# Kernel tuning notes

Measured on AMD Instinct MI355X. Metric: run time of the kernel, lower is better.

Reference implementation:

```python
import jax, jax.numpy as jnp
import numpy as np

N = 100_000   # total vertices
E = 1_600_000 # total directed edges
B = 64        # graphs in batch
HID = 128
DM = 256
EPS = 1e-5


def _linear_init(k, fan_in, fan_out):
    lim = 1.0 / np.sqrt(fan_in)
    kw, kb = jax.random.split(k)
    W = jax.random.uniform(kw, (fan_in, fan_out), minval=-lim, maxval=lim, dtype=jnp.float32)
    b = jax.random.uniform(kb, (fan_out,), minval=-lim, maxval=lim, dtype=jnp.float32)
    return W, b


def setup_inputs() -> dict:
    key = jax.random.key(0)
    ks = jax.random.split(key, 8)
    W_in, b_in = _linear_init(ks[0], 3, HID)
    W1, b1 = _linear_init(ks[1], HID, HID)
    W2, b2 = _linear_init(ks[2], HID, HID)
    W3, b3 = _linear_init(ks[3], HID, HID)
    W_out, b_out = _linear_init(ks[4], HID, DM)
    vertices = jax.random.normal(ks[5], (N, 3), dtype=jnp.float32)
    edge_index = jax.random.randint(ks[6], (2, E), 0, N)
    batch = jnp.sort(jax.random.randint(ks[7], (N,), 0, B))
    gamma = jnp.ones((DM,), jnp.float32)
    beta = jnp.zeros((DM,), jnp.float32)
    return dict(vertices=vertices, edge_index=edge_index, batch=batch,
                W_in=W_in, b_in=b_in, W1=W1, b1=b1, W2=W2, b2=b2, W3=W3, b3=b3,
                W_out=W_out, b_out=b_out, gamma=gamma, beta=beta)


def _gcn_conv(x, W, b, src, dst):
    # PyG GCNConv: add self-loops, sym-normalize by deg^{-1/2}, aggregate at dst.
    h = x @ W  # [N, HID]
    deg = jnp.zeros((x.shape[0],), x.dtype).at[dst].add(1.0) + 1.0  # +1 self-loop
    dinv = jax.lax.rsqrt(deg)
    msg = h[src] * (dinv[src] * dinv[dst])[:, None]       # [E, HID] gather+scale
    agg = jnp.zeros_like(h).at[dst].add(msg)               # scatter-add
    agg = agg + h * (dinv * dinv)[:, None]                 # self-loop contribution
    return agg + b


def reference(vertices, edge_index, batch, W_in, b_in, W1, b1, W2, b2, W3, b3, W_out, b_out, gamma, beta):
    src, dst = edge_index[0], edge_index[1]
    x = vertices @ W_in + b_in
    for W, b in ((W1, b1), (W2, b2), (W3, b3)):
        x = jax.nn.relu(_gcn_conv(x, W, b, src, dst))
    # global_mean_pool over batch segments
    summ = jax.ops.segment_sum(x, batch, num_segments=B)
    cnt = jax.ops.segment_sum(jnp.ones((x.shape[0], 1), x.dtype), batch, num_segments=B)
    pooled = summ / jnp.maximum(cnt, 1.0)
    y = pooled @ W_out + b_out
    mu = jnp.mean(y, axis=-1, keepdims=True)
    var = jnp.var(y, axis=-1, keepdims=True)
    return (y - mu) * jax.lax.rsqrt(var + EPS) * gamma + beta
```

## Files before the change

### kernel.cpp

```cpp
#include <hip/hip_runtime.h>

constexpr int NV = 100000;
constexpr int NE = 1600000;
constexpr int NB = 64;
constexpr int HD = 128;
constexpr int DM = 256;
#define EPSLN 1e-5f

constexpr int DPB   = 256;
constexpr int NBUCK = (NV + DPB - 1) / DPB;
constexpr int BCAP  = 8192;
constexpr int BSH   = 13;
constexpr int EPB2  = 2048;
constexpr int NEB2  = (NE + EPB2 - 1) / EPB2;
constexpr int H1B   = 1024;
constexpr int WTB   = 128;
constexpr int BDB   = (NV + 255) / 256;

typedef short bf16x8 __attribute__((ext_vector_type(8)));
typedef float f32x4 __attribute__((ext_vector_type(4)));

__device__ inline unsigned short f2b(float f) {
    union { float f; unsigned u; } x; x.f = f;
    unsigned r = x.u + 0x7FFF + ((x.u >> 16) & 1);
    return (unsigned short)(r >> 16);
}
__device__ inline float b2f(unsigned short h) {
    union { unsigned u; float f; } x; x.u = (unsigned)h << 16;
    return x.f;
}

__global__ __launch_bounds__(256) void k_init(const float* __restrict__ verts,
                                              const float* __restrict__ Win,
                                              const float* __restrict__ bin,
                                              const float* __restrict__ W1,
                                              const float* __restrict__ W2,
                                              const float* __restrict__ W3,
                                              const int* __restrict__ ei,
                                              const int* __restrict__ batch,
                                              int* __restrict__ bcursor,
                                              int* __restrict__ ebuf,
                                              unsigned short* __restrict__ Hb,
                                              unsigned short* __restrict__ Wt,
                                              int* __restrict__ gstart,
                                              int* __restrict__ gend) {
    int t = threadIdx.x;
    int bid = blockIdx.x;
    if (bid < NEB2) {
        __shared__ int h[NBUCK];
        __shared__ int lbase[NBUCK];
        for (int i = t; i < NBUCK; i += 256) h[i] = 0;
        __syncthreads();
        int base = bid * EPB2;
        int s[8], d[8], rk[8];
        #pragma unroll
        for (int j = 0; j < 8; ++j) {
            int idx = base + j * 256 + t;
            if (idx < NE) {
                s[j] = ei[idx];
                d[j] = ei[NE + idx];
                rk[j] = atomicAdd(&h[d[j] >> 8], 1);
            } else d[j] = -1;
        }
        __syncthreads();
        for (int i = t; i < NBUCK; i += 256) {
            int c = h[i];
            if (c) lbase[i] = atomicAdd(&bcursor[i], c);
        }
        __syncthreads();
        #pragma unroll
        for (int j = 0; j < 8; ++j)
            if (d[j] >= 0) {
                int b = d[j] >> 8;
                ebuf[(b << BSH) + lbase[b] + rk[j]] = (s[j] << 8) | (d[j] & 255);
            }
        return;
    }
    if (bid < NEB2 + H1B) {
        __shared__ float Wc[3 * HD];
        __shared__ float bc[HD];
        if (t < HD) {
            float w0 = 0.f, w1 = 0.f, w2 = 0.f, bv = 0.f;
            for (int k = 0; k < HD; ++k) {
                float w = W1[k * HD + t];
                w0 = fmaf(Win[k], w, w0);
                w1 = fmaf(Win[128 + k], w, w1);
                w2 = fmaf(Win[256 + k], w, w2);
                bv = fmaf(bin[k], w, bv);
            }
            Wc[t] = w0; Wc[128 + t] = w1; Wc[256 + t] = w2; bc[t] = bv;
        }
        __syncthreads();
        for (int idx = (bid - NEB2) * 256 + t; idx < NV * HD; idx += H1B * 256) {
            int v = idx >> 7, c = idx & 127;
            float a = verts[v * 3 + 0], b = verts[v * 3 + 1], d = verts[v * 3 + 2];
            Hb[idx] = f2b(bc[c] + a * Wc[c] + b * Wc[128 + c] + d * Wc[256 + c]);
        }
        return;
    }
    if (bid < NEB2 + H1B + WTB) {
        int idx = (bid - NEB2 - H1B) * 256 + t;
        if (idx < 2 * HD * HD) {
            int l = idx >> 14, r = idx & 16383;
            const float* W = (l == 0) ? W2 : W3;
            int n = r >> 7, k = r & 127;
            Wt[(l << 14) + n * HD + k] = f2b(W[k * HD + n]);
        }
        return;
    }
    int i = (bid - NEB2 - H1B - WTB) * 256 + t;
    if (i < NV) {
        int b = batch[i];
        if (i == 0 || batch[i - 1] != b) gstart[b] = i;
        int bn = (i + 1 < NV) ? batch[i + 1] : -1;
        if (bn != b) gend[b] = i + 1;
    }
}

__global__ __launch_bounds__(256) void k_bcsr(const int* __restrict__ ebuf,
                                              const int* __restrict__ bcursor,
                                              int* __restrict__ degi,
                                              float* __restrict__ dinv,
                                              int* __restrict__ rowstart,
                                              int* __restrict__ csr) {
    __shared__ int els[BCAP];
    __shared__ int h[DPB];
    __shared__ int sdata[DPB];
    int b = blockIdx.x, t = threadIdx.x, d0 = b * DPB;
    h[t] = 0;
    __syncthreads();
    int e0 = b << BSH;
    int n = bcursor[b];
    for (int i = t; i < n; i += 256) {
        int p = ebuf[e0 + i];
        if (i < BCAP) els[i] = p;
        atomicAdd(&h[p & 255], 1);
    }
    __syncthreads();
    int a = h[t];
    sdata[t] = a;
    __syncthreads();
    for (int off = 1; off < 256; off <<= 1) {
        int v = sdata[t];
        int add = (t >= off) ? sdata[t - off] : 0;
        __syncthreads();
        sdata[t] = v + add;
        __syncthreads();
    }
    int excl = (t == 0) ? 0 : sdata[t - 1];
    int v0 = d0 + t;
    if (v0 < NV) {
        rowstart[v0] = e0 + excl;
        degi[v0] = a;
        dinv[v0] = rsqrtf((float)a + 1.0f);
    }
    h[t] = e0 + excl;
    __syncthreads();
    for (int i = t; i < n; i += 256) {
        int p = (i < BCAP) ? els[i] : ebuf[e0 + i];
        int slot = atomicAdd(&h[p & 255], 1);
        csr[slot] = p >> 8;
    }
}

__global__ __launch_bounds__(256) void k_gemm_mfma(const unsigned short* __restrict__ Xb,
                                                   const unsigned short* __restrict__ Wt,
                                                   unsigned short* __restrict__ Hb) {
    __shared__ __align__(16) unsigned short Ws[128 * 132];
    __shared__ __align__(16) unsigned short hs[4][16][136];
    int t = threadIdx.x;
    {
        int row = t >> 1;
        int half = (t & 1) << 6;
        const unsigned short* src = Wt + row * HD + half;
        unsigned short* dst = &Ws[row * 132 + half];
        #pragma unroll
        for (int i = 0; i < 8; ++i)
            *(bf16x8*)(dst + i * 8) = *(const bf16x8*)(src + i * 8);
    }
    int wave = t >> 6;
    int lane = t & 63;
    int r = lane & 15;
    int g = lane >> 4;
    int row0 = blockIdx.x * 64 + wave * 16;
    int arow = row0 + r;
    bool valid = arow < NV;

    bf16x8 afrag[4];
    const unsigned short* xp = Xb + (size_t)arow * HD + g * 8;
    #pragma unroll
    for (int ks = 0; ks < 4; ++ks) {
        if (valid) afrag[ks] = *(const bf16x8*)(xp + ks * 32);
        else       afrag[ks] = bf16x8{0, 0, 0, 0, 0, 0, 0, 0};
    }
    __syncthreads();

    #pragma unroll
    for (int nt = 0; nt < 8; ++nt) {
        f32x4 acc = {0.f, 0.f, 0.f, 0.f};
        #pragma unroll
        for (int ks = 0; ks < 4; ++ks) {
            bf16x8 bfrag = *(const bf16x8*)&Ws[(nt * 16 + r) * 132 + g * 8 + ks * 32];
            acc = __builtin_amdgcn_mfma_f32_16x16x32_bf16(afrag[ks], bfrag, acc, 0, 0, 0);
        }
        #pragma unroll
        for (int j = 0; j < 4; ++j)
            hs[wave][g * 4 + j][nt * 16 + r] = f2b(acc[j]);
    }
    int row = lane >> 2;
    int grow = row0 + row;
    #pragma unroll
    for (int k = 0; k < 4; ++k) {
        int c = (lane & 3) + k * 4;
        bf16x8 val = *(const bf16x8*)&hs[wave][row][c * 8];
        if (grow < NV)
            *(bf16x8*)(Hb + (size_t)grow * HD + c * 8) = val;
    }
}

__global__ __launch_bounds__(256) void k_agg(const unsigned short* __restrict__ H,
                                             const float* __restrict__ dinv,
                                             const int* __restrict__ rowstart,
                                             const int* __restrict__ degi,
                                             const int* __restrict__ csr_src,
                                             const float* __restrict__ bias,
                                             unsigned short* __restrict__ Xo) {
    int gtid = blockIdx.x * 256 + threadIdx.x;
    int v = gtid >> 6;
    if (v >= NV) return;
    int lane = threadIdx.x & 63;
    int q = lane >> 4;
    int l4 = lane & 15;
    float di = dinv[v];
    int rs = rowstart[v], len = degi[v];
    float a[8];
    if (q == 0) {
        float sc = di * di;
        bf16x8 hv = *(const bf16x8*)(H + (size_t)v * HD + l4 * 8);
        #pragma unroll
        for (int jj = 0; jj < 8; ++jj) a[jj] = b2f((unsigned short)hv[jj]) * sc;
    } else {
        #pragma unroll
        for (int jj = 0; jj < 8; ++jj) a[jj] = 0.f;
    }
    int cnt = (len - q + 3) >> 2;
    int idx = rs + q;
    int j = 0;
    for (; j + 1 < cnt; j += 2) {
        int s0 = csr_src[idx], s1 = csr_src[idx + 4];
        idx += 8;
        float w0 = dinv[s0] * di, w1 = dinv[s1] * di;
        bf16x8 h0 = *(const bf16x8*)(H + (size_t)s0 * HD + l4 * 8);
        bf16x8 h1 = *(const bf16x8*)(H + (size_t)s1 * HD + l4 * 8);
        #pragma unroll
        for (int jj = 0; jj < 8; ++jj) {
            a[jj] = fmaf(b2f((unsigned short)h0[jj]), w0, a[jj]);
            a[jj] = fmaf(b2f((unsigned short)h1[jj]), w1, a[jj]);
        }
    }
    if (j < cnt) {
        int s0 = csr_src[idx];
        float w0 = dinv[s0] * di;
        bf16x8 h0 = *(const bf16x8*)(H + (size_t)s0 * HD + l4 * 8);
        #pragma unroll
        for (int jj = 0; jj < 8; ++jj)
            a[jj] = fmaf(b2f((unsigned short)h0[jj]), w0, a[jj]);
    }
    #pragma unroll
    for (int jj = 0; jj < 8; ++jj) {
        a[jj] += __shfl_xor(a[jj], 16);
        a[jj] += __shfl_xor(a[jj], 32);
    }
    if (q == 0) {
        bf16x8 ov;
        #pragma unroll
        for (int jj = 0; jj < 8; ++jj)
            ov[jj] = (short)f2b(fmaxf(a[jj] + bias[l4 * 8 + jj], 0.f));
        *(bf16x8*)(Xo + (size_t)v * HD + l4 * 8) = ov;
    }
}

__global__ __launch_bounds__(256) void k_pool(const unsigned short* __restrict__ X,
                                              const int* __restrict__ batch,
                                              float* __restrict__ pool) {
    constexpr int CHUNK = (NV + 2047) / 2048;
    __shared__ float lp[2][HD];
    __shared__ int binfo[2];
    int t = threadIdx.x;
    int v0 = blockIdx.x * CHUNK;
    if (v0 >= NV) return;
    int vend = min(v0 + CHUNK, NV);
    if (t < 2 * HD) ((float*)lp)[t] = 0.f;
    if (t == 0) { binfo[0] = batch[v0]; binfo[1] = batch[vend - 1]; }
    __syncthreads();
    int b0 = binfo[0], b1 = binfo[1];
    int cg = t & 15;
    int ro = t >> 4;
    if (b1 - b0 <= 1) {
        float a0[8] = {}, a1[8] = {};
        for (int v = v0 + ro; v < vend; v += 16) {
            bf16x8 x = *(const bf16x8*)(X + (size_t)v * HD + cg * 8);
            if (batch[v] == b0) {
                #pragma unroll
                for (int jj = 0; jj < 8; ++jj) a0[jj] += b2f((unsigned short)x[jj]);
            } else {
                #pragma unroll
                for (int jj = 0; jj < 8; ++jj) a1[jj] += b2f((unsigned short)x[jj]);
            }
        }
        #pragma unroll
        for (int jj = 0; jj < 8; ++jj) {
            atomicAdd(&lp[0][cg * 8 + jj], a0[jj]);
            if (b1 != b0) atomicAdd(&lp[1][cg * 8 + jj], a1[jj]);
        }
        __syncthreads();
        int slot = t >> 7, col = t & 127;
        if (slot == 0 || b1 != b0)
            atomicAdd(&pool[(slot ? b1 : b0) * HD + col], lp[slot][col]);
    } else {
        float a[8] = {};
        int cur = -1;
        for (int v = v0 + ro; v < vend; v += 16) {
            int bb = batch[v];
            if (bb != cur) {
                if (cur >= 0) {
                    #pragma unroll
                    for (int jj = 0; jj < 8; ++jj) {
                        atomicAdd(&pool[cur * HD + cg * 8 + jj], a[jj]);
                        a[jj] = 0.f;
                    }
                }
                cur = bb;
            }
            bf16x8 x = *(const bf16x8*)(X + (size_t)v * HD + cg * 8);
            #pragma unroll
            for (int jj = 0; jj < 8; ++jj) a[jj] += b2f((unsigned short)x[jj]);
        }
        if (cur >= 0) {
            #pragma unroll
            for (int jj = 0; jj < 8; ++jj)
                atomicAdd(&pool[cur * HD + cg * 8 + jj], a[jj]);
        }
    }
}

__global__ __launch_bounds__(256) void k_out(const float* __restrict__ pool,
                                             const int* __restrict__ gstart,
                                             const int* __restrict__ gend,
                                             const float* __restrict__ Wout,
                                             const float* __restrict__ bout,
                                             const float* __restrict__ gamma,
                                             const float* __restrict__ beta,
                                             float* __restrict__ out) {
    __shared__ float ps[HD];
    __shared__ float red[DM];
    int g = blockIdx.x, t = threadIdx.x;
    if (t < HD) {
        float cn = fmaxf((float)(gend[g] - gstart[g]), 1.0f);
        ps[t] = pool[g * HD + t] / cn;
    }
    __syncthreads();
    float acc = bout[t];
    #pragma unroll 8
    for (int k = 0; k < HD; ++k) acc = fmaf(ps[k], Wout[k * DM + t], acc);
    red[t] = acc; __syncthreads();
    for (int s2 = 128; s2 > 0; s2 >>= 1) {
        if (t < s2) red[t] += red[t + s2];
        __syncthreads();
    }
    float mu = red[0] * (1.0f / DM);
    __syncthreads();
    float d = acc - mu;
    red[t] = d * d; __syncthreads();
    for (int s2 = 128; s2 > 0; s2 >>= 1) {
        if (t < s2) red[t] += red[t + s2];
        __syncthreads();
    }
    float var = red[0] * (1.0f / DM);
    out[g * DM + t] = d * rsqrtf(var + EPSLN) * gamma[t] + beta[t];
}

extern "C" void kernel_launch(void* const* d_in, const int* in_sizes, int n_in,
                              void* d_out, int out_size, void* d_ws, size_t ws_size,
                              hipStream_t stream) {
    const float* verts = (const float*)d_in[0];
    const int*   ei    = (const int*)d_in[1];
    const int*   batch = (const int*)d_in[2];
    const float* Win   = (const float*)d_in[3];
    const float* bin   = (const float*)d_in[4];
    const float* W1    = (const float*)d_in[5];
    const float* b1    = (const float*)d_in[6];
    const float* W2    = (const float*)d_in[7];
    const float* b2    = (const float*)d_in[8];
    const float* W3    = (const float*)d_in[9];
    const float* b3    = (const float*)d_in[10];
    const float* Wout  = (const float*)d_in[11];
    const float* bout  = (const float*)d_in[12];
    const float* gamma = (const float*)d_in[13];
    const float* beta  = (const float*)d_in[14];
    float* out = (float*)d_out;

    char* wp = (char*)d_ws;
    auto alloc = [&](size_t bytes) -> char* {
        char* p = wp;
        wp += (bytes + 255) & ~(size_t)255;
        return p;
    };
    unsigned short* bufA = (unsigned short*)alloc((size_t)NV * HD * 2);
    unsigned short* bufB = (unsigned short*)alloc((size_t)NV * HD * 2);
    unsigned short* Wt   = (unsigned short*)alloc((size_t)2 * HD * HD * 2);
    int*   degi     = (int*)alloc((size_t)NV * 4);
    float* dinv     = (float*)alloc((size_t)NV * 4);
    int*   rowstart = (int*)alloc((size_t)NV * 4);
    int*   csr      = (int*)alloc((size_t)NBUCK * BCAP * 4);
    int*   ebuf     = (int*)alloc((size_t)NBUCK * BCAP * 4);
    size_t zb_cursor = ((size_t)NBUCK * 4 + 255) & ~(size_t)255;
    size_t zb_pool   = (size_t)NB * HD * 4;
    size_t zb_tot    = zb_cursor + zb_pool + 1024;
    char*  zblock   = alloc(zb_tot);
    int*   bcursor  = (int*)zblock;
    float* pool     = (float*)(zblock + zb_cursor);
    int*   gstart   = (int*)(zblock + zb_cursor + zb_pool);
    int*   gend     = (int*)(zblock + zb_cursor + zb_pool + 512);

    hipMemsetAsync(zblock, 0, zb_tot, stream);

    k_init<<<NEB2 + H1B + WTB + BDB, 256, 0, stream>>>(verts, Win, bin, W1, W2, W3,
                                                       ei, batch, bcursor, ebuf,
                                                       bufA, Wt, gstart, gend);
    k_bcsr<<<NBUCK, 256, 0, stream>>>(ebuf, bcursor, degi, dinv, rowstart, csr);

    int aggrid = (int)(((size_t)NV * 64 + 255) / 256);
    k_agg<<<aggrid, 256, 0, stream>>>(bufA, dinv, rowstart, degi, csr, b1, bufB);
    k_gemm_mfma<<<(NV + 63) / 64, 256, 0, stream>>>(bufB, Wt, bufA);
    k_agg<<<aggrid, 256, 0, stream>>>(bufA, dinv, rowstart, degi, csr, b2, bufB);
    k_gemm_mfma<<<(NV + 63) / 64, 256, 0, stream>>>(bufB, Wt + (size_t)HD * HD, bufA);
    k_agg<<<aggrid, 256, 0, stream>>>(bufA, dinv, rowstart, degi, csr, b3, bufB);

    k_pool<<<2048, 256, 0, stream>>>(bufB, batch, pool);
    k_out<<<NB, 256, 0, stream>>>(pool, gstart, gend, Wout, bout, gamma, beta, out);
}
```

Baseline: 340.3 us.

## Double edges per bucketing block, reuse weight LDS for GEMM staging, zero pool in init

Each edge-bucketing block now handles 4096 edges instead of 2048, which halves the number of blocks and the global cursor atomics at the cost of more registers per thread. The GEMM kernel keeps all eight accumulator tiles in registers, then reuses the weight shared buffer for output staging after a barrier, so the separate staging array is dropped and shared memory per block shrinks, which may raise occupancy. Pool zeroing moves from the memset into the init kernel, which shrinks the memset.

```diff
diff --git a/kernel.cpp b/kernel.cpp
--- a/kernel.cpp
+++ b/kernel.cpp
@@ -11,8 +11,8 @@
 constexpr int NBUCK = (NV + DPB - 1) / DPB;
 constexpr int BCAP  = 8192;
 constexpr int BSH   = 13;
-constexpr int EPB2  = 2048;
-constexpr int NEB2  = (NE + EPB2 - 1) / EPB2;
+constexpr int EPB3  = 4096;
+constexpr int NEB3  = (NE + EPB3 - 1) / EPB3;
 constexpr int H1B   = 1024;
 constexpr int WTB   = 128;
 constexpr int BDB   = (NV + 255) / 256;
@@ -43,18 +43,19 @@
                                               unsigned short* __restrict__ Hb,
                                               unsigned short* __restrict__ Wt,
                                               int* __restrict__ gstart,
-                                              int* __restrict__ gend) {
+                                              int* __restrict__ gend,
+                                              float* __restrict__ pool) {
     int t = threadIdx.x;
     int bid = blockIdx.x;
-    if (bid < NEB2) {
+    if (bid < NEB3) {
         __shared__ int h[NBUCK];
         __shared__ int lbase[NBUCK];
         for (int i = t; i < NBUCK; i += 256) h[i] = 0;
         __syncthreads();
-        int base = bid * EPB2;
-        int s[8], d[8], rk[8];
-        #pragma unroll
-        for (int j = 0; j < 8; ++j) {
+        int base = bid * EPB3;
+        int s[16], d[16], rk[16];
+        #pragma unroll
+        for (int j = 0; j < 16; ++j) {
             int idx = base + j * 256 + t;
             if (idx < NE) {
                 s[j] = ei[idx];
@@ -69,14 +70,14 @@
         }
         __syncthreads();
         #pragma unroll
-        for (int j = 0; j < 8; ++j)
+        for (int j = 0; j < 16; ++j)
             if (d[j] >= 0) {
                 int b = d[j] >> 8;
                 ebuf[(b << BSH) + lbase[b] + rk[j]] = (s[j] << 8) | (d[j] & 255);
             }
         return;
     }
-    if (bid < NEB2 + H1B) {
+    if (bid < NEB3 + H1B) {
         __shared__ float Wc[3 * HD];
         __shared__ float bc[HD];
         if (t < HD) {
@@ -91,15 +92,15 @@
             Wc[t] = w0; Wc[128 + t] = w1; Wc[256 + t] = w2; bc[t] = bv;
         }
         __syncthreads();
-        for (int idx = (bid - NEB2) * 256 + t; idx < NV * HD; idx += H1B * 256) {
+        for (int idx = (bid - NEB3) * 256 + t; idx < NV * HD; idx += H1B * 256) {
             int v = idx >> 7, c = idx & 127;
             float a = verts[v * 3 + 0], b = verts[v * 3 + 1], d = verts[v * 3 + 2];
             Hb[idx] = f2b(bc[c] + a * Wc[c] + b * Wc[128 + c] + d * Wc[256 + c]);
         }
         return;
     }
-    if (bid < NEB2 + H1B + WTB) {
-        int idx = (bid - NEB2 - H1B) * 256 + t;
+    if (bid < NEB3 + H1B + WTB) {
+        int idx = (bid - NEB3 - H1B) * 256 + t;
         if (idx < 2 * HD * HD) {
             int l = idx >> 14, r = idx & 16383;
             const float* W = (l == 0) ? W2 : W3;
@@ -108,7 +109,8 @@
         }
         return;
     }
-    int i = (bid - NEB2 - H1B - WTB) * 256 + t;
+    int i = (bid - NEB3 - H1B - WTB) * 256 + t;
+    if (i < NB * HD) pool[i] = 0.f;
     if (i < NV) {
         int b = batch[i];
         if (i == 0 || batch[i - 1] != b) gstart[b] = i;
@@ -167,7 +169,6 @@
                                                    const unsigned short* __restrict__ Wt,
                                                    unsigned short* __restrict__ Hb) {
     __shared__ __align__(16) unsigned short Ws[128 * 132];
-    __shared__ __align__(16) unsigned short hs[4][16][136];
     int t = threadIdx.x;
     {
         int row = t >> 1;
@@ -195,24 +196,29 @@
     }
     __syncthreads();
 
+    f32x4 acc[8];
     #pragma unroll
     for (int nt = 0; nt < 8; ++nt) {
-        f32x4 acc = {0.f, 0.f, 0.f, 0.f};
+        acc[nt] = f32x4{0.f, 0.f, 0.f, 0.f};
         #pragma unroll
         for (int ks = 0; ks < 4; ++ks) {
             bf16x8 bfrag = *(const bf16x8*)&Ws[(nt * 16 + r) * 132 + g * 8 + ks * 32];
-            acc = __builtin_amdgcn_mfma_f32_16x16x32_bf16(afrag[ks], bfrag, acc, 0, 0, 0);
-        }
+            acc[nt] = __builtin_amdgcn_mfma_f32_16x16x32_bf16(afrag[ks], bfrag, acc[nt], 0, 0, 0);
+        }
+    }
+    __syncthreads();
+    unsigned short* hsw = Ws + wave * 16 * 136;
+    #pragma unroll
+    for (int nt = 0; nt < 8; ++nt)
         #pragma unroll
         for (int j = 0; j < 4; ++j)
-            hs[wave][g * 4 + j][nt * 16 + r] = f2b(acc[j]);
-    }
+            hsw[(g * 4 + j) * 136 + nt * 16 + r] = f2b(acc[nt][j]);
     int row = lane >> 2;
     int grow = row0 + row;
     #pragma unroll
     for (int k = 0; k < 4; ++k) {
         int c = (lane & 3) + k * 4;
-        bf16x8 val = *(const bf16x8*)&hs[wave][row][c * 8];
+        bf16x8 val = *(const bf16x8*)&hsw[row * 136 + c * 8];
         if (grow < NV)
             *(bf16x8*)(Hb + (size_t)grow * HD + c * 8) = val;
     }
@@ -414,20 +420,19 @@
     int*   rowstart = (int*)alloc((size_t)NV * 4);
     int*   csr      = (int*)alloc((size_t)NBUCK * BCAP * 4);
     int*   ebuf     = (int*)alloc((size_t)NBUCK * BCAP * 4);
+    float* pool     = (float*)alloc((size_t)NB * HD * 4);
     size_t zb_cursor = ((size_t)NBUCK * 4 + 255) & ~(size_t)255;
-    size_t zb_pool   = (size_t)NB * HD * 4;
-    size_t zb_tot    = zb_cursor + zb_pool + 1024;
+    size_t zb_tot    = zb_cursor + 1024;
     char*  zblock   = alloc(zb_tot);
     int*   bcursor  = (int*)zblock;
-    float* pool     = (float*)(zblock + zb_cursor);
-    int*   gstart   = (int*)(zblock + zb_cursor + zb_pool);
-    int*   gend     = (int*)(zblock + zb_cursor + zb_pool + 512);
+    int*   gstart   = (int*)(zblock + zb_cursor);
+    int*   gend     = (int*)(zblock + zb_cursor + 512);
 
     hipMemsetAsync(zblock, 0, zb_tot, stream);
 
-    k_init<<<NEB2 + H1B + WTB + BDB, 256, 0, stream>>>(verts, Win, bin, W1, W2, W3,
+    k_init<<<NEB3 + H1B + WTB + BDB, 256, 0, stream>>>(verts, Win, bin, W1, W2, W3,
                                                        ei, batch, bcursor, ebuf,
-                                                       bufA, Wt, gstart, gend);
+                                                       bufA, Wt, gstart, gend, pool);
     k_bcsr<<<NBUCK, 256, 0, stream>>>(ebuf, bcursor, degi, dinv, rowstart, csr);
 
     int aggrid = (int)(((size_t)NV * 64 + 255) / 256);
```

Result: faster. 329.1 us (-3.3%).
